# Optimization experiments

Measured on AMD Instinct MI355X. Metric: run time of the kernel, lower is better.

Reference implementation:

```python
import jax, jax.numpy as jnp
import numpy as np

N_Q, N_KV, DIM, D_K, D_V = 4096, 4096, 1024, 1024, 1024

def setup_inputs() -> dict:
    key = jax.random.key(0)
    ks = jax.random.split(key, 6)
    return {
        "q": jax.random.normal(ks[0], (N_Q, DIM), dtype=jnp.float32),
        "k": jax.random.normal(ks[1], (N_KV, DIM), dtype=jnp.float32),
        "v": jax.random.normal(ks[2], (N_KV, DIM), dtype=jnp.float32),
        "W_q": jax.random.uniform(ks[3], (DIM, D_K), dtype=jnp.float32),
        "W_k": jax.random.uniform(ks[4], (DIM, D_V), dtype=jnp.float32),
        "W_v": jax.random.uniform(ks[5], (DIM, D_V), dtype=jnp.float32),
    }

def reference(q, k, v, W_q, W_k, W_v) -> jnp.ndarray:
    d_k = W_q.shape[1]
    Q = q @ W_q                      # (n, d_k)
    K = k @ W_k                      # (N, d_v)
    V = v @ W_v                      # (N, d_v)
    scores = (Q @ K.T) / jnp.sqrt(jnp.asarray(d_k, Q.dtype))  # (n, N)
    attn = jax.nn.softmax(scores, axis=-1)
    return attn @ V                  # (n, d_v)
```

## Files before the change

kernel.cpp:

```cpp
#include <hip/hip_runtime.h>
#include <hip/hip_bf16.h>
#include <stdint.h>

typedef float  f32x4  __attribute__((ext_vector_type(4)));
typedef short  s16x8  __attribute__((ext_vector_type(8)));
typedef unsigned short u16;

#define BK 32

__device__ inline u16 f32_to_bf16_rn(float f) {
  uint32_t u = __builtin_bit_cast(uint32_t, f);
  u += 0x7FFFu + ((u >> 16) & 1u);
  return (u16)(u >> 16);
}
__device__ inline float bf16u_to_f32(u16 h) {
  uint32_t u = ((uint32_t)h) << 16;
  return __builtin_bit_cast(float, u);
}
__device__ inline void split2(float x, u16& hi, u16& lo) {
  u16 h = f32_to_bf16_rn(x);
  lo = f32_to_bf16_rn(x - bf16u_to_f32(h));
  hi = h;
}

__device__ inline void stage16(const u16* g, u16* l) {
  __builtin_amdgcn_global_load_lds((const __attribute__((address_space(1))) uint32_t*)g,
                                   (__attribute__((address_space(3))) uint32_t*)l,
                                   16, 0, 0);
}

__device__ inline void xcd_swz(int& bx, int& by) {
  int nx = gridDim.x, nwg = nx * gridDim.y;
  if ((nwg & 7) == 0) {
    int wg = blockIdx.x + nx * blockIdx.y;
    int s = (wg & 7) * (nwg >> 3) + (wg >> 3);
    bx = s % nx;
    by = s / nx;
  } else {
    bx = blockIdx.x;
    by = blockIdx.y;
  }
}


__global__ __launch_bounds__(256) void split_rows3(const float* __restrict__ in0,
                                                   const float* __restrict__ in1,
                                                   const float* __restrict__ in2,
                                                   u16* __restrict__ hi0, u16* __restrict__ lo0,
                                                   u16* __restrict__ hi1, u16* __restrict__ lo1,
                                                   u16* __restrict__ hi2, u16* __restrict__ lo2,
                                                   int n4) {
  int i = blockIdx.x * 256 + threadIdx.x;
  if (i >= n4) return;
  const float* in = blockIdx.z == 0 ? in0 : blockIdx.z == 1 ? in1 : in2;
  u16* hi = blockIdx.z == 0 ? hi0 : blockIdx.z == 1 ? hi1 : hi2;
  u16* lo = blockIdx.z == 0 ? lo0 : blockIdx.z == 1 ? lo1 : lo2;
  float4 t = ((const float4*)in)[i];
  ushort4 h, l;
  split2(t.x, h.x, l.x);
  split2(t.y, h.y, l.y);
  split2(t.z, h.z, l.z);
  split2(t.w, h.w, l.w);
  ((ushort4*)hi)[i] = h;
  ((ushort4*)lo)[i] = l;
}

__global__ __launch_bounds__(256) void split_transpose3(const float* __restrict__ in0,
                                                        const float* __restrict__ in1,
                                                        const float* __restrict__ in2,
                                                        u16* __restrict__ thi0, u16* __restrict__ tlo0,
                                                        u16* __restrict__ thi1, u16* __restrict__ tlo1,
                                                        u16* __restrict__ thi2, u16* __restrict__ tlo2,
                                                        int R, int C) {
  const float* in = blockIdx.z == 0 ? in0 : blockIdx.z == 1 ? in1 : in2;
  u16* thi = blockIdx.z == 0 ? thi0 : blockIdx.z == 1 ? thi1 : thi2;
  u16* tlo = blockIdx.z == 0 ? tlo0 : blockIdx.z == 1 ? tlo1 : tlo2;
  __shared__ float tile[32][33];
  int tx = threadIdx.x & 31, ty = threadIdx.x >> 5;
  int r0 = blockIdx.y * 32, c0 = blockIdx.x * 32;
#pragma unroll
  for (int j = 0; j < 32; j += 8)
    tile[ty + j][tx] = in[(size_t)(r0 + ty + j) * C + c0 + tx];
  __syncthreads();
#pragma unroll
  for (int j = 0; j < 32; j += 8) {
    float x = tile[tx][ty + j];
    u16 h, l;
    split2(x, h, l);
    size_t o = (size_t)(c0 + ty + j) * R + r0 + tx;
    thi[o] = h;
    tlo[o] = l;
  }
}

__global__ __launch_bounds__(256) void transpose_u16_2(const u16* __restrict__ in0,
                                                       const u16* __restrict__ in1,
                                                       u16* __restrict__ out0,
                                                       u16* __restrict__ out1, int R, int C) {
  const u16* in = blockIdx.z == 0 ? in0 : in1;
  u16* out = blockIdx.z == 0 ? out0 : out1;
  __shared__ u16 tile[32][33];
  int tx = threadIdx.x & 31, ty = threadIdx.x >> 5;
  int r0 = blockIdx.y * 32, c0 = blockIdx.x * 32;
#pragma unroll
  for (int j = 0; j < 32; j += 8)
    tile[ty + j][tx] = in[(size_t)(r0 + ty + j) * C + c0 + tx];
  __syncthreads();
#pragma unroll
  for (int j = 0; j < 32; j += 8)
    out[(size_t)(c0 + ty + j) * R + r0 + tx] = tile[tx][ty + j];
}

__global__ __launch_bounds__(256) void add_inplace2(float* __restrict__ a,
                                                    const float* __restrict__ b,
                                                    const float* __restrict__ c, int n4) {
  int i = blockIdx.x * 256 + threadIdx.x;
  if (i >= n4) return;
  float4 x = ((const float4*)a)[i];
  float4 y = ((const float4*)b)[i];
  float4 z = ((const float4*)c)[i];
  x.x += y.x + z.x;
  x.y += y.y + z.y;
  x.z += y.z + z.z;
  x.w += y.w + z.w;
  ((float4*)a)[i] = x;
}

template <int TBM, int TBN, int OUT_SPLIT>
__device__ __forceinline__ void gemm_body(
    const u16* __restrict__ Ahi, const u16* __restrict__ Alo, int lda,
    const u16* __restrict__ Bhi, const u16* __restrict__ Blo, int ldb,
    float* __restrict__ Cf, u16* __restrict__ Chi, u16* __restrict__ Clo, int ldc,
    int Kdim, int k0, float scale, int arow0, int bcol0) {
  constexpr int WTM = TBM / 2, WTN = TBN / 2;
  constexpr int FM = WTM / 16, FN = WTN / 16;
  constexpr int CA = TBM * BK / 8 / 256;
  constexpr int CB = TBN * BK / 8 / 256;

  __shared__ alignas(16) u16 sAh[TBM * BK];
  __shared__ alignas(16) u16 sAl[TBM * BK];
  __shared__ alignas(16) u16 sBh[TBN * BK];
  __shared__ alignas(16) u16 sBl[TBN * BK];

  const int tid = threadIdx.x;
  const int lane = tid & 63;
  const int wid = tid >> 6;
  const int wr = wid >> 1, wc = wid & 1;

  const u16* gAh[CA];
  const u16* gAl[CA];
  int ldsA[CA];
#pragma unroll
  for (int i = 0; i < CA; ++i) {
    int c = tid + i * 256;
    int r = c >> 2, k8 = (c & 3) * 8;
    gAh[i] = Ahi + (size_t)(arow0 + r) * lda + k0 + k8;
    gAl[i] = Alo + (size_t)(arow0 + r) * lda + k0 + k8;
    ldsA[i] = c * 8;
  }
  const u16* gBh[CB];
  const u16* gBl[CB];
  int ldsB[CB];
#pragma unroll
  for (int i = 0; i < CB; ++i) {
    int c = tid + i * 256;
    int r = c >> 2, k8 = (c & 3) * 8;
    gBh[i] = Bhi + (size_t)(bcol0 + r) * ldb + k0 + k8;
    gBl[i] = Blo + (size_t)(bcol0 + r) * ldb + k0 + k8;
    ldsB[i] = c * 8;
  }

  f32x4 acc[FM][FN];
#pragma unroll
  for (int m = 0; m < FM; ++m)
#pragma unroll
    for (int n = 0; n < FN; ++n) acc[m][n] = (f32x4)0.0f;

  const int frow = lane & 15;
  const int fk = (lane >> 4) * 8;
  const int aoff = (wr * WTM + frow) * BK + fk;
  const int boff = (wc * WTN + frow) * BK + fk;

  for (int kt = 0; kt < Kdim; kt += BK) {
#pragma unroll
    for (int i = 0; i < CA; ++i) {
      stage16(gAh[i], &sAh[ldsA[i]]);
      stage16(gAl[i], &sAl[ldsA[i]]);
      gAh[i] += BK;
      gAl[i] += BK;
    }
#pragma unroll
    for (int i = 0; i < CB; ++i) {
      stage16(gBh[i], &sBh[ldsB[i]]);
      stage16(gBl[i], &sBl[ldsB[i]]);
      gBh[i] += BK;
      gBl[i] += BK;
    }
    __syncthreads();

    s16x8 ah[FM], al[FM], bh[FN], bl[FN];
#pragma unroll
    for (int m = 0; m < FM; ++m) {
      ah[m] = *(const s16x8*)&sAh[aoff + m * 16 * BK];
      al[m] = *(const s16x8*)&sAl[aoff + m * 16 * BK];
    }
#pragma unroll
    for (int n = 0; n < FN; ++n) {
      bh[n] = *(const s16x8*)&sBh[boff + n * 16 * BK];
      bl[n] = *(const s16x8*)&sBl[boff + n * 16 * BK];
    }
#pragma unroll
    for (int m = 0; m < FM; ++m)
#pragma unroll
      for (int n = 0; n < FN; ++n) {
        acc[m][n] = __builtin_amdgcn_mfma_f32_16x16x32_bf16(ah[m], bh[n], acc[m][n], 0, 0, 0);
        acc[m][n] = __builtin_amdgcn_mfma_f32_16x16x32_bf16(ah[m], bl[n], acc[m][n], 0, 0, 0);
        acc[m][n] = __builtin_amdgcn_mfma_f32_16x16x32_bf16(al[m], bh[n], acc[m][n], 0, 0, 0);
      }
    __syncthreads();
  }

  const int rbase = arow0 + wr * WTM + (lane >> 4) * 4;
  const int cbase = bcol0 + wc * WTN + frow;
#pragma unroll
  for (int m = 0; m < FM; ++m)
#pragma unroll
    for (int n = 0; n < FN; ++n)
#pragma unroll
      for (int r = 0; r < 4; ++r) {
        int row = rbase + m * 16 + r;
        int col = cbase + n * 16;
        float val = acc[m][n][r] * scale;
        if (OUT_SPLIT) {
          u16 h, l;
          split2(val, h, l);
          Chi[(size_t)row * ldc + col] = h;
          Clo[(size_t)row * ldc + col] = l;
        } else {
          Cf[(size_t)row * ldc + col] = val;
        }
      }
}

template <int TBM, int TBN, int OUT_SPLIT>
__global__ __launch_bounds__(256, 2) void gemm_bt_x3(
    const u16* __restrict__ Ahi, const u16* __restrict__ Alo, int lda,
    const u16* __restrict__ Bhi, const u16* __restrict__ Blo, int ldb,
    float* __restrict__ Cf, u16* __restrict__ Chi, u16* __restrict__ Clo, int ldc,
    int Kdim, float scale) {
  int bx, by;
  xcd_swz(bx, by);
  gemm_body<TBM, TBN, OUT_SPLIT>(Ahi, Alo, lda, Bhi, Blo, ldb, Cf, Chi, Clo, ldc,
                                 Kdim, 0, scale, by * TBM, bx * TBN);
}

__global__ __launch_bounds__(256, 2) void proj3(
    const u16* __restrict__ a0h, const u16* __restrict__ a0l,
    const u16* __restrict__ a1h, const u16* __restrict__ a1l,
    const u16* __restrict__ a2h, const u16* __restrict__ a2l,
    const u16* __restrict__ b0h, const u16* __restrict__ b0l,
    const u16* __restrict__ b1h, const u16* __restrict__ b1l,
    const u16* __restrict__ b2h, const u16* __restrict__ b2l,
    u16* __restrict__ c0h, u16* __restrict__ c0l,
    u16* __restrict__ c1h, u16* __restrict__ c1l,
    u16* __restrict__ c2h, u16* __restrict__ c2l,
    int D, float scale0) {
  const int z = blockIdx.z;
  const u16* Ah = z == 0 ? a0h : z == 1 ? a1h : a2h;
  const u16* Al = z == 0 ? a0l : z == 1 ? a1l : a2l;
  const u16* Bh = z == 0 ? b0h : z == 1 ? b1h : b2h;
  const u16* Bl = z == 0 ? b0l : z == 1 ? b1l : b2l;
  u16* Ch = z == 0 ? c0h : z == 1 ? c1h : c2h;
  u16* Cl = z == 0 ? c0l : z == 1 ? c1l : c2l;
  float scale = z == 0 ? scale0 : 1.0f;
  int bx, by;
  xcd_swz(bx, by);
  gemm_body<64, 128, 1>(Ah, Al, D, Bh, Bl, D, nullptr, Ch, Cl, D,
                        D, 0, scale, by * 64, bx * 128);
}

__global__ __launch_bounds__(256, 2) void gemm_pv_splitk3(
    const u16* __restrict__ Ahi, const u16* __restrict__ Alo, int lda,
    const u16* __restrict__ Bhi, const u16* __restrict__ Blo, int ldb,
    float* __restrict__ Cf0, float* __restrict__ Cf1, float* __restrict__ Cf2, int ldc) {
  const int z = blockIdx.z;
  float* Cf = z == 0 ? Cf0 : z == 1 ? Cf1 : Cf2;
  const int k0 = z == 0 ? 0 : 1344 + (z - 1) * 1376;
  const int kd = z == 0 ? 1344 : 1376;
  int bx, by;
  xcd_swz(bx, by);
  gemm_body<64, 128, 0>(Ahi, Alo, lda, Bhi, Blo, ldb, Cf, nullptr, nullptr, ldc,
                        kd, k0, 1.0f, by * 64, bx * 128);
}

__global__ __launch_bounds__(256) void softmax_rows(float* __restrict__ S, int N) {
  const int tid = threadIdx.x;
  float* row = S + (size_t)blockIdx.x * N;
  const float4* row4 = (const float4*)row;
  float v[16];
#pragma unroll
  for (int i = 0; i < 4; ++i) {
    float4 t = row4[tid + i * 256];
    v[i * 4 + 0] = t.x;
    v[i * 4 + 1] = t.y;
    v[i * 4 + 2] = t.z;
    v[i * 4 + 3] = t.w;
  }
  float m = -__builtin_inff();
#pragma unroll
  for (int i = 0; i < 16; ++i) m = fmaxf(m, v[i]);
#pragma unroll
  for (int o = 32; o > 0; o >>= 1) m = fmaxf(m, __shfl_xor(m, o));
  __shared__ float redm[4];
  __shared__ float reds[4];
  const int wid = tid >> 6;
  if ((tid & 63) == 0) redm[wid] = m;
  __syncthreads();
  m = fmaxf(fmaxf(redm[0], redm[1]), fmaxf(redm[2], redm[3]));

  float s = 0.f;
#pragma unroll
  for (int i = 0; i < 16; ++i) {
    v[i] = __expf(v[i] - m);
    s += v[i];
  }
#pragma unroll
  for (int o = 32; o > 0; o >>= 1) s += __shfl_xor(s, o);
  if ((tid & 63) == 0) reds[wid] = s;
  __syncthreads();
  s = reds[0] + reds[1] + reds[2] + reds[3];
  float inv = 1.0f / s;

  u16* hrow = (u16*)row;
  u16* lrow = hrow + N;
#pragma unroll
  for (int i = 0; i < 4; ++i) {
    ushort4 h4, l4;
    split2(v[i * 4 + 0] * inv, h4.x, l4.x);
    split2(v[i * 4 + 1] * inv, h4.y, l4.y);
    split2(v[i * 4 + 2] * inv, h4.z, l4.z);
    split2(v[i * 4 + 3] * inv, h4.w, l4.w);
    ((ushort4*)hrow)[tid + i * 256] = h4;
    ((ushort4*)lrow)[tid + i * 256] = l4;
  }
}

extern "C" void kernel_launch(void* const* d_in, const int* in_sizes, int n_in,
                              void* d_out, int out_size, void* d_ws, size_t ws_size,
                              hipStream_t stream) {
  (void)in_sizes; (void)n_in; (void)out_size; (void)ws_size;
  const float* q  = (const float*)d_in[0];
  const float* k  = (const float*)d_in[1];
  const float* v  = (const float*)d_in[2];
  const float* Wq = (const float*)d_in[3];
  const float* Wk = (const float*)d_in[4];
  const float* Wv = (const float*)d_in[5];
  float* out = (float*)d_out;

  char* ws = (char*)d_ws;
  const size_t MB = 1ull << 20;
  u16* q_hi = (u16*)(ws + 0 * MB);
  u16* q_lo = (u16*)(ws + 8 * MB);
  u16* k_hi = (u16*)(ws + 16 * MB);
  u16* k_lo = (u16*)(ws + 24 * MB);
  u16* v_hi = (u16*)(ws + 32 * MB);
  u16* v_lo = (u16*)(ws + 40 * MB);
  u16* V_hi = (u16*)(ws + 48 * MB);
  u16* V_lo = (u16*)(ws + 56 * MB);
  float* S  = (float*)(ws + 0 * MB);
  u16* WqT_hi = (u16*)(ws + 64 * MB);
  u16* WqT_lo = (u16*)(ws + 66 * MB);
  u16* WkT_hi = (u16*)(ws + 68 * MB);
  u16* WkT_lo = (u16*)(ws + 70 * MB);
  u16* WvT_hi = (u16*)(ws + 72 * MB);
  u16* WvT_lo = (u16*)(ws + 74 * MB);
  u16* Q_hi = (u16*)(ws + 76 * MB);
  u16* Q_lo = (u16*)(ws + 84 * MB);
  u16* K_hi = (u16*)(ws + 92 * MB);
  u16* K_lo = (u16*)(ws + 100 * MB);
  u16* VT_hi = (u16*)(ws + 108 * MB);
  u16* VT_lo = (u16*)(ws + 116 * MB);
  float* PVp1 = (float*)(ws + 76 * MB);
  float* PVp2 = (float*)(ws + 92 * MB);

  const int NQ = 4096, NKV = 4096, D = 1024;

  int n4 = NQ * D / 4;
  split_rows3<<<dim3(n4 / 256, 1, 3), 256, 0, stream>>>(q, k, v, q_hi, q_lo, k_hi, k_lo,
                                                        v_hi, v_lo, n4);

  split_transpose3<<<dim3(D / 32, D / 32, 3), 256, 0, stream>>>(
      Wq, Wk, Wv, WqT_hi, WqT_lo, WkT_hi, WkT_lo, WvT_hi, WvT_lo, D, D);

  proj3<<<dim3(D / 128, NQ / 64, 3), 256, 0, stream>>>(
      q_hi, q_lo, k_hi, k_lo, v_hi, v_lo,
      WqT_hi, WqT_lo, WkT_hi, WkT_lo, WvT_hi, WvT_lo,
      Q_hi, Q_lo, K_hi, K_lo, V_hi, V_lo, D, 0.03125f);

  transpose_u16_2<<<dim3(D / 32, NKV / 32, 2), 256, 0, stream>>>(V_hi, V_lo, VT_hi, VT_lo,
                                                                 NKV, D);

  dim3 gs(NKV / 128, NQ / 128);
  gemm_bt_x3<128, 128, 0><<<gs, 256, 0, stream>>>(Q_hi, Q_lo, D, K_hi, K_lo, D,
                                                  S, nullptr, nullptr, NKV, D, 1.0f);

  softmax_rows<<<NQ, 256, 0, stream>>>(S, NKV);

  gemm_pv_splitk3<<<dim3(D / 128, NQ / 64, 3), 256, 0, stream>>>(
      (u16*)S, (u16*)S + NKV, 2 * NKV, VT_hi, VT_lo, NKV, out, PVp1, PVp2, D);

  add_inplace2<<<NQ * D / 4 / 256, 256, 0, stream>>>(out, PVp1, PVp2, NQ * D / 4);
}
```

Before: 464.6 us.

## Rewrite split-bf16 GEMMs as 512-thread double-buffered pipelined kernels with swizzled LDS

Replaces the generic 256-thread GEMM body with an 8-wave, 256-row-tile kernel. It double-buffers LDS, issues next-tile global-to-LDS loads spread across compute phases, XOR-swizzles the LDS layout to avoid bank conflicts, and raises wave priority around the MFMA blocks. The projection, scores and PV GEMMs all use the new body. PV split-K drops from three pieces to two, so the reduction kernel reads one partial instead of two. The goal is to hide global load latency behind MFMA work and raise data reuse per tile. The cost is heavier register and LDS use per block and fewer blocks in flight for PV.

```diff
diff --git a/kernel.cpp b/kernel.cpp
--- a/kernel.cpp
+++ b/kernel.cpp
@@ -23,9 +23,9 @@
   hi = h;
 }
 
-__device__ inline void stage16(const u16* g, u16* l) {
+__device__ inline void stage16(const u16* g, const u16* l) {
   __builtin_amdgcn_global_load_lds((const __attribute__((address_space(1))) uint32_t*)g,
-                                   (__attribute__((address_space(3))) uint32_t*)l,
+                                   (__attribute__((address_space(3))) uint32_t*)(u16*)l,
                                    16, 0, 0);
 }
 
@@ -111,126 +111,141 @@
     out[(size_t)(c0 + ty + j) * R + r0 + tx] = tile[tx][ty + j];
 }
 
-__global__ __launch_bounds__(256) void add_inplace2(float* __restrict__ a,
-                                                    const float* __restrict__ b,
-                                                    const float* __restrict__ c, int n4) {
+__global__ __launch_bounds__(256) void add_inplace(float* __restrict__ a,
+                                                   const float* __restrict__ b, int n4) {
   int i = blockIdx.x * 256 + threadIdx.x;
   if (i >= n4) return;
   float4 x = ((const float4*)a)[i];
   float4 y = ((const float4*)b)[i];
-  float4 z = ((const float4*)c)[i];
-  x.x += y.x + z.x;
-  x.y += y.y + z.y;
-  x.z += y.z + z.z;
-  x.w += y.w + z.w;
+  x.x += y.x; x.y += y.y; x.z += y.z; x.w += y.w;
   ((float4*)a)[i] = x;
 }
 
-template <int TBM, int TBN, int OUT_SPLIT>
-__device__ __forceinline__ void gemm_body(
+template <int TBN, int OUT_SPLIT>
+__device__ __forceinline__ void gemm8p_body(
     const u16* __restrict__ Ahi, const u16* __restrict__ Alo, int lda,
     const u16* __restrict__ Bhi, const u16* __restrict__ Blo, int ldb,
     float* __restrict__ Cf, u16* __restrict__ Chi, u16* __restrict__ Clo, int ldc,
-    int Kdim, int k0, float scale, int arow0, int bcol0) {
-  constexpr int WTM = TBM / 2, WTN = TBN / 2;
-  constexpr int FM = WTM / 16, FN = WTN / 16;
-  constexpr int CA = TBM * BK / 8 / 256;
-  constexpr int CB = TBN * BK / 8 / 256;
-
-  __shared__ alignas(16) u16 sAh[TBM * BK];
-  __shared__ alignas(16) u16 sAl[TBM * BK];
-  __shared__ alignas(16) u16 sBh[TBN * BK];
-  __shared__ alignas(16) u16 sBl[TBN * BK];
+    int NT, int k0, float scale, int arow0, int bcol0) {
+  constexpr int NW = TBN / 4;
+  constexpr int FN = NW / 16;
+  constexpr int NCA = 256 * 8;
+  constexpr int NCB = TBN * 8;
+  constexpr int TISS = (NCA + NCB) / 512;
+  constexpr int H1 = (TISS + 1) / 2;
+  constexpr int BB = NCA * 8;
+
+  __shared__ alignas(16) u16 lds[2][(NCA + NCB) * 8];
 
   const int tid = threadIdx.x;
   const int lane = tid & 63;
   const int wid = tid >> 6;
-  const int wr = wid >> 1, wc = wid & 1;
-
-  const u16* gAh[CA];
-  const u16* gAl[CA];
-  int ldsA[CA];
-#pragma unroll
-  for (int i = 0; i < CA; ++i) {
-    int c = tid + i * 256;
-    int r = c >> 2, k8 = (c & 3) * 8;
-    gAh[i] = Ahi + (size_t)(arow0 + r) * lda + k0 + k8;
-    gAl[i] = Alo + (size_t)(arow0 + r) * lda + k0 + k8;
-    ldsA[i] = c * 8;
-  }
-  const u16* gBh[CB];
-  const u16* gBl[CB];
-  int ldsB[CB];
-#pragma unroll
-  for (int i = 0; i < CB; ++i) {
-    int c = tid + i * 256;
-    int r = c >> 2, k8 = (c & 3) * 8;
-    gBh[i] = Bhi + (size_t)(bcol0 + r) * ldb + k0 + k8;
-    gBl[i] = Blo + (size_t)(bcol0 + r) * ldb + k0 + k8;
-    ldsB[i] = c * 8;
-  }
-
-  f32x4 acc[FM][FN];
-#pragma unroll
-  for (int m = 0; m < FM; ++m)
+  const int wr = wid >> 2;
+  const int wc = wid & 3;
+  const int frow = lane & 15;
+  const int koct = lane >> 4;
+
+  const u16* src[TISS];
+  int loff[TISS];
+#pragma unroll
+  for (int j = 0; j < TISS; ++j) {
+    int g = j * 512 + wid * 64 + lane;
+    loff[j] = g * 8;
+    if (g < NCA) {
+      int r = g >> 3, ch = g & 7, c2 = ch ^ (r & 7);
+      const u16* base = (c2 < 4) ? Ahi : Alo;
+      src[j] = base + (size_t)(arow0 + r) * lda + k0 + (c2 & 3) * 8;
+    } else {
+      int gb = g - NCA;
+      int r = gb >> 3, ch = gb & 7, c2 = ch ^ (r & 7);
+      const u16* base = (c2 < 4) ? Bhi : Blo;
+      src[j] = base + (size_t)(bcol0 + r) * ldb + k0 + (c2 & 3) * 8;
+    }
+  }
+
+  f32x4 acc[8][FN];
+#pragma unroll
+  for (int m = 0; m < 8; ++m)
 #pragma unroll
     for (int n = 0; n < FN; ++n) acc[m][n] = (f32x4)0.0f;
 
-  const int frow = lane & 15;
-  const int fk = (lane >> 4) * 8;
-  const int aoff = (wr * WTM + frow) * BK + fk;
-  const int boff = (wc * WTN + frow) * BK + fk;
-
-  for (int kt = 0; kt < Kdim; kt += BK) {
-#pragma unroll
-    for (int i = 0; i < CA; ++i) {
-      stage16(gAh[i], &sAh[ldsA[i]]);
-      stage16(gAl[i], &sAl[ldsA[i]]);
-      gAh[i] += BK;
-      gAl[i] += BK;
+#pragma unroll
+  for (int j = 0; j < TISS; ++j) stage16(src[j], &lds[0][loff[j]]);
+#pragma unroll
+  for (int j = 0; j < TISS; ++j) src[j] += BK;
+  asm volatile("s_waitcnt vmcnt(0)" ::: "memory");
+  __builtin_amdgcn_sched_barrier(0);
+  __builtin_amdgcn_s_barrier();
+
+  for (int t = 0; t < NT; ++t) {
+    const u16* cur = lds[t & 1];
+    const u16* nxt = lds[(t + 1) & 1];
+    const bool st = (t + 1 < NT);
+    s16x8 bh[FN], bl[FN];
+#pragma unroll
+    for (int p = 0; p < 4; ++p) {
+      s16x8 ah[2], al[2];
+      if (p == 0) {
+#pragma unroll
+        for (int n = 0; n < FN; ++n) {
+          int br = wc * NW + n * 16 + frow;
+          bh[n] = *(const s16x8*)&cur[BB + br * 64 + ((koct ^ (br & 7)) << 3)];
+          bl[n] = *(const s16x8*)&cur[BB + br * 64 + (((4 | koct) ^ (br & 7)) << 3)];
+        }
+      }
+#pragma unroll
+      for (int m = 0; m < 2; ++m) {
+        int ar = wr * 128 + p * 32 + m * 16 + frow;
+        ah[m] = *(const s16x8*)&cur[ar * 64 + ((koct ^ (ar & 7)) << 3)];
+        al[m] = *(const s16x8*)&cur[ar * 64 + (((4 | koct) ^ (ar & 7)) << 3)];
+      }
+      if (st && p == 0) {
+#pragma unroll
+        for (int j = 0; j < H1; ++j) stage16(src[j], &nxt[loff[j]]);
+      }
+      if (st && p == 1) {
+#pragma unroll
+        for (int j = H1; j < TISS; ++j) stage16(src[j], &nxt[loff[j]]);
+#pragma unroll
+        for (int j = 0; j < TISS; ++j) src[j] += BK;
+      }
+      __builtin_amdgcn_sched_barrier(0);
+      __builtin_amdgcn_s_barrier();
+      asm volatile("s_waitcnt lgkmcnt(0)" ::: "memory");
+      __builtin_amdgcn_sched_barrier(0);
+      __builtin_amdgcn_s_setprio(1);
+#pragma unroll
+      for (int m = 0; m < 2; ++m)
+#pragma unroll
+        for (int n = 0; n < FN; ++n) {
+          acc[p * 2 + m][n] =
+              __builtin_amdgcn_mfma_f32_16x16x32_bf16(ah[m], bh[n], acc[p * 2 + m][n], 0, 0, 0);
+          acc[p * 2 + m][n] =
+              __builtin_amdgcn_mfma_f32_16x16x32_bf16(ah[m], bl[n], acc[p * 2 + m][n], 0, 0, 0);
+          acc[p * 2 + m][n] =
+              __builtin_amdgcn_mfma_f32_16x16x32_bf16(al[m], bh[n], acc[p * 2 + m][n], 0, 0, 0);
+        }
+      __builtin_amdgcn_s_setprio(0);
+      __builtin_amdgcn_sched_barrier(0);
+      if (p == 3) {
+        asm volatile("s_waitcnt vmcnt(0)" ::: "memory");
+        __builtin_amdgcn_sched_barrier(0);
+      }
+      __builtin_amdgcn_s_barrier();
     }
-#pragma unroll
-    for (int i = 0; i < CB; ++i) {
-      stage16(gBh[i], &sBh[ldsB[i]]);
-      stage16(gBl[i], &sBl[ldsB[i]]);
-      gBh[i] += BK;
-      gBl[i] += BK;
-    }
-    __syncthreads();
-
-    s16x8 ah[FM], al[FM], bh[FN], bl[FN];
-#pragma unroll
-    for (int m = 0; m < FM; ++m) {
-      ah[m] = *(const s16x8*)&sAh[aoff + m * 16 * BK];
-      al[m] = *(const s16x8*)&sAl[aoff + m * 16 * BK];
-    }
-#pragma unroll
-    for (int n = 0; n < FN; ++n) {
-      bh[n] = *(const s16x8*)&sBh[boff + n * 16 * BK];
-      bl[n] = *(const s16x8*)&sBl[boff + n * 16 * BK];
-    }
-#pragma unroll
-    for (int m = 0; m < FM; ++m)
-#pragma unroll
-      for (int n = 0; n < FN; ++n) {
-        acc[m][n] = __builtin_amdgcn_mfma_f32_16x16x32_bf16(ah[m], bh[n], acc[m][n], 0, 0, 0);
-        acc[m][n] = __builtin_amdgcn_mfma_f32_16x16x32_bf16(ah[m], bl[n], acc[m][n], 0, 0, 0);
-        acc[m][n] = __builtin_amdgcn_mfma_f32_16x16x32_bf16(al[m], bh[n], acc[m][n], 0, 0, 0);
-      }
-    __syncthreads();
-  }
-
-  const int rbase = arow0 + wr * WTM + (lane >> 4) * 4;
-  const int cbase = bcol0 + wc * WTN + frow;
-#pragma unroll
-  for (int m = 0; m < FM; ++m)
+  }
+
+  const int rb = arow0 + wr * 128 + koct * 4;
+  const int cb = bcol0 + wc * NW + frow;
+#pragma unroll
+  for (int mg = 0; mg < 8; ++mg)
 #pragma unroll
     for (int n = 0; n < FN; ++n)
 #pragma unroll
       for (int r = 0; r < 4; ++r) {
-        int row = rbase + m * 16 + r;
-        int col = cbase + n * 16;
-        float val = acc[m][n][r] * scale;
+        int row = rb + mg * 16 + r;
+        int col = cb + n * 16;
+        float val = acc[mg][n][r] * scale;
         if (OUT_SPLIT) {
           u16 h, l;
           split2(val, h, l);
@@ -242,19 +257,17 @@
       }
 }
 
-template <int TBM, int TBN, int OUT_SPLIT>
-__global__ __launch_bounds__(256, 2) void gemm_bt_x3(
+__global__ __launch_bounds__(512, 2) void scores8p(
     const u16* __restrict__ Ahi, const u16* __restrict__ Alo, int lda,
     const u16* __restrict__ Bhi, const u16* __restrict__ Blo, int ldb,
-    float* __restrict__ Cf, u16* __restrict__ Chi, u16* __restrict__ Clo, int ldc,
-    int Kdim, float scale) {
+    float* __restrict__ Cf, int ldc, int NT, float scale) {
   int bx, by;
   xcd_swz(bx, by);
-  gemm_body<TBM, TBN, OUT_SPLIT>(Ahi, Alo, lda, Bhi, Blo, ldb, Cf, Chi, Clo, ldc,
-                                 Kdim, 0, scale, by * TBM, bx * TBN);
-}
-
-__global__ __launch_bounds__(256, 2) void proj3(
+  gemm8p_body<256, 0>(Ahi, Alo, lda, Bhi, Blo, ldb, Cf, nullptr, nullptr, ldc,
+                      NT, 0, scale, by * 256, bx * 256);
+}
+
+__global__ __launch_bounds__(512, 2) void proj8p(
     const u16* __restrict__ a0h, const u16* __restrict__ a0l,
     const u16* __restrict__ a1h, const u16* __restrict__ a1l,
     const u16* __restrict__ a2h, const u16* __restrict__ a2l,
@@ -275,22 +288,19 @@
   float scale = z == 0 ? scale0 : 1.0f;
   int bx, by;
   xcd_swz(bx, by);
-  gemm_body<64, 128, 1>(Ah, Al, D, Bh, Bl, D, nullptr, Ch, Cl, D,
-                        D, 0, scale, by * 64, bx * 128);
-}
-
-__global__ __launch_bounds__(256, 2) void gemm_pv_splitk3(
+  gemm8p_body<128, 1>(Ah, Al, D, Bh, Bl, D, nullptr, Ch, Cl, D,
+                      D / BK, 0, scale, by * 256, bx * 128);
+}
+
+__global__ __launch_bounds__(512, 2) void pv8p(
     const u16* __restrict__ Ahi, const u16* __restrict__ Alo, int lda,
     const u16* __restrict__ Bhi, const u16* __restrict__ Blo, int ldb,
-    float* __restrict__ Cf0, float* __restrict__ Cf1, float* __restrict__ Cf2, int ldc) {
-  const int z = blockIdx.z;
-  float* Cf = z == 0 ? Cf0 : z == 1 ? Cf1 : Cf2;
-  const int k0 = z == 0 ? 0 : 1344 + (z - 1) * 1376;
-  const int kd = z == 0 ? 1344 : 1376;
+    float* __restrict__ Cf0, float* __restrict__ Cf1, int ldc, int KH) {
+  float* Cf = blockIdx.z == 0 ? Cf0 : Cf1;
   int bx, by;
   xcd_swz(bx, by);
-  gemm_body<64, 128, 0>(Ahi, Alo, lda, Bhi, Blo, ldb, Cf, nullptr, nullptr, ldc,
-                        kd, k0, 1.0f, by * 64, bx * 128);
+  gemm8p_body<128, 0>(Ahi, Alo, lda, Bhi, Blo, ldb, Cf, nullptr, nullptr, ldc,
+                      KH / BK, blockIdx.z * KH, 1.0f, by * 256, bx * 128);
 }
 
 __global__ __launch_bounds__(256) void softmax_rows(float* __restrict__ S, int N) {
@@ -381,7 +391,6 @@
   u16* VT_hi = (u16*)(ws + 108 * MB);
   u16* VT_lo = (u16*)(ws + 116 * MB);
   float* PVp1 = (float*)(ws + 76 * MB);
-  float* PVp2 = (float*)(ws + 92 * MB);
 
   const int NQ = 4096, NKV = 4096, D = 1024;
 
@@ -392,7 +401,7 @@
   split_transpose3<<<dim3(D / 32, D / 32, 3), 256, 0, stream>>>(
       Wq, Wk, Wv, WqT_hi, WqT_lo, WkT_hi, WkT_lo, WvT_hi, WvT_lo, D, D);
 
-  proj3<<<dim3(D / 128, NQ / 64, 3), 256, 0, stream>>>(
+  proj8p<<<dim3(D / 128, NQ / 256, 3), 512, 0, stream>>>(
       q_hi, q_lo, k_hi, k_lo, v_hi, v_lo,
       WqT_hi, WqT_lo, WkT_hi, WkT_lo, WvT_hi, WvT_lo,
       Q_hi, Q_lo, K_hi, K_lo, V_hi, V_lo, D, 0.03125f);
@@ -400,14 +409,13 @@
   transpose_u16_2<<<dim3(D / 32, NKV / 32, 2), 256, 0, stream>>>(V_hi, V_lo, VT_hi, VT_lo,
                                                                  NKV, D);
 
-  dim3 gs(NKV / 128, NQ / 128);
-  gemm_bt_x3<128, 128, 0><<<gs, 256, 0, stream>>>(Q_hi, Q_lo, D, K_hi, K_lo, D,
-                                                  S, nullptr, nullptr, NKV, D, 1.0f);
+  scores8p<<<dim3(NKV / 256, NQ / 256), 512, 0, stream>>>(Q_hi, Q_lo, D, K_hi, K_lo, D,
+                                                          S, NKV, D / BK, 1.0f);
 
   softmax_rows<<<NQ, 256, 0, stream>>>(S, NKV);
 
-  gemm_pv_splitk3<<<dim3(D / 128, NQ / 64, 3), 256, 0, stream>>>(
-      (u16*)S, (u16*)S + NKV, 2 * NKV, VT_hi, VT_lo, NKV, out, PVp1, PVp2, D);
-
-  add_inplace2<<<NQ * D / 4 / 256, 256, 0, stream>>>(out, PVp1, PVp2, NQ * D / 4);
-}
+  pv8p<<<dim3(D / 128, NQ / 256, 2), 512, 0, stream>>>(
+      (u16*)S, (u16*)S + NKV, 2 * NKV, VT_hi, VT_lo, NKV, out, PVp1, D, NKV / 2);
+
+  add_inplace<<<NQ * D / 4 / 256, 256, 0, stream>>>(out, PVp1, NQ * D / 4);
+}
```

New measurement: 405.5 us. -12.7%, faster.
